# Kernel optimization log

Hardware: AMD Instinct MI355X
Metric: run time of the kernel (lower is better)

The kernel has to match this reference:

```python
import jax, jax.numpy as jnp
import numpy as np

B, O, A, H, Z = 4096, 512, 64, 2048, 256
CLAMP = 10.0


def _lin(x, w, b):
    # torch nn.Linear layout: w [out, in]
    return x @ w.T + b


def setup_inputs() -> dict:
    key = jax.random.key(0)
    ks = jax.random.split(key, 24)
    n = jax.random.normal
    s = 0.02
    inp = {
        'x_t': n(ks[0], (B, O), jnp.float32),
        'a_prev': n(ks[1], (B, A), jnp.float32),
        'h_prev': n(ks[2], (B, H), jnp.float32),
        'eps': n(ks[3], (B, Z), jnp.float32),
        # prior_net: Linear(H,H) -> ReLU -> Linear(H, 2Z)
        'prior_w1': n(ks[4], (H, H), jnp.float32) * s,
        'prior_b1': jnp.zeros((H,), jnp.float32),
        'prior_w2': n(ks[5], (2 * Z, H), jnp.float32) * s,
        'prior_b2': jnp.zeros((2 * Z,), jnp.float32),
        # enc_net: Linear(O+H,H) -> ReLU -> Linear(H, 2Z)
        'enc_w1': n(ks[6], (H, O + H), jnp.float32) * s,
        'enc_b1': jnp.zeros((H,), jnp.float32),
        'enc_w2': n(ks[7], (2 * Z, H), jnp.float32) * s,
        'enc_b2': jnp.zeros((2 * Z,), jnp.float32),
        # dec_net: Linear(Z+H,H) -> ReLU -> Linear(H, 2O)
        'dec_w1': n(ks[8], (H, Z + H), jnp.float32) * s,
        'dec_b1': jnp.zeros((H,), jnp.float32),
        'dec_w2': n(ks[9], (2 * O, H), jnp.float32) * s,
        'dec_b2': jnp.zeros((2 * O,), jnp.float32),
        # GRUCell: input = O + A + Z, gates ordered (r, z, n)
        'w_ih': n(ks[10], (3 * H, O + A + Z), jnp.float32) * s,
        'w_hh': n(ks[11], (3 * H, H), jnp.float32) * s,
        'b_ih': jnp.zeros((3 * H,), jnp.float32),
        'b_hh': jnp.zeros((3 * H,), jnp.float32),
    }
    return inp


def vrnn_step(x_t, a_prev, h_prev, eps,
              prior_w1, prior_b1, prior_w2, prior_b2,
              enc_w1, enc_b1, enc_w2, enc_b2,
              dec_w1, dec_b1, dec_w2, dec_b2,
              w_ih, w_hh, b_ih, b_hh):
    # prior stats from h_prev
    prior_stats = _lin(jax.nn.relu(_lin(h_prev, prior_w1, prior_b1)), prior_w2, prior_b2)
    mu_p, logvar_p = jnp.split(prior_stats, 2, axis=-1)

    # encoder on [x, h]
    enc_stats = _lin(jax.nn.relu(_lin(jnp.concatenate([x_t, h_prev], -1), enc_w1, enc_b1)), enc_w2, enc_b2)
    mu_q, logvar_q = jnp.split(enc_stats, 2, axis=-1)
    logvar_q = jnp.clip(logvar_q, -CLAMP, CLAMP)
    std_q = jnp.exp(0.5 * logvar_q)
    z_t = mu_q + eps * std_q  # reparameterization

    # decoder on [z, h]
    dec_out = _lin(jax.nn.relu(_lin(jnp.concatenate([z_t, h_prev], -1), dec_w1, dec_b1)), dec_w2, dec_b2)
    mu_x, logvar_x = jnp.split(dec_out, 2, axis=-1)
    logvar_x = jnp.clip(logvar_x, -CLAMP, CLAMP)
    nll = 0.5 * jnp.sum((x_t - mu_x) ** 2 * jnp.exp(-logvar_x) + logvar_x, axis=-1)

    # KL(q || p), diagonal Gaussians
    var_p = jnp.exp(logvar_p)
    kl = 0.5 * jnp.sum((mu_q - mu_p) ** 2 / var_p + jnp.exp(logvar_q) / var_p
                       + (logvar_p - logvar_q) - 1.0, axis=-1)

    # GRUCell (torch gate order: r, z, n)
    rnn_in = jnp.concatenate([x_t, z_t, a_prev], -1)
    gi = rnn_in @ w_ih.T + b_ih
    gh = h_prev @ w_hh.T + b_hh
    i_r, i_z, i_n = jnp.split(gi, 3, axis=-1)
    h_r, h_z, h_n = jnp.split(gh, 3, axis=-1)
    r = jax.nn.sigmoid(i_r + h_r)
    zg = jax.nn.sigmoid(i_z + h_z)
    n = jnp.tanh(i_n + r * h_n)
    h_t = (1.0 - zg) * n + zg * h_prev

    return h_t, nll, kl, z_t, mu_q, logvar_q


def reference(x_t, a_prev, h_prev, eps,
              prior_w1, prior_b1, prior_w2, prior_b2,
              enc_w1, enc_b1, enc_w2, enc_b2,
              dec_w1, dec_b1, dec_w2, dec_b2,
              w_ih, w_hh, b_ih, b_hh):
    return vrnn_step(x_t, a_prev, h_prev, eps,
                     prior_w1, prior_b1, prior_w2, prior_b2,
                     enc_w1, enc_b1, enc_w2, enc_b2,
                     dec_w1, dec_b1, dec_w2, dec_b2,
                     w_ih, w_hh, b_ih, b_hh)
```

## Files before the change

kernel.cpp:

```cpp
#include <hip/hip_runtime.h>
#include <stdint.h>


#define B_SZ 4096
#define H_SZ 2048
#define Z_SZ 256

typedef __attribute__((ext_vector_type(4))) float f32x4;
typedef __attribute__((ext_vector_type(8))) short s16x8;

__device__ __forceinline__ uint16_t f2b(float f) {
  union { float f; uint32_t u; } v; v.f = f;
  uint32_t u = v.u;
  uint32_t r = (u + 0x7FFFu + ((u >> 16) & 1u)) >> 16;
  return (uint16_t)r;
}
__device__ __forceinline__ float b2f(uint16_t h) {
  union { uint32_t u; float f; } v; v.u = ((uint32_t)h) << 16; return v.f;
}
__device__ __forceinline__ float clip10(float v) { return fminf(fmaxf(v, -10.0f), 10.0f); }

struct MC {
  const float* src[14];
  uint16_t* dst[14];
  int c8[14];
  int sld[14];
  int dld[14];
  int base[15];
};

__global__ __launch_bounds__(256) void multiconv(MC mc, int nseg, int total) {
  int gid = blockIdx.x * 256 + threadIdx.x;
  if (gid >= total) return;
  int s = 0;
  while (s + 1 < nseg && gid >= mc.base[s + 1]) ++s;
  int local = gid - mc.base[s];
  int c8 = mc.c8[s];
  int row = local / c8;
  int cg = local - row * c8;
  const f32x4* sp = (const f32x4*)(mc.src[s] + (size_t)row * mc.sld[s] + (size_t)cg * 8);
  f32x4 lo = sp[0], hi = sp[1];
  s16x8 p;
  p[0] = (short)f2b(lo[0]); p[1] = (short)f2b(lo[1]);
  p[2] = (short)f2b(lo[2]); p[3] = (short)f2b(lo[3]);
  p[4] = (short)f2b(hi[0]); p[5] = (short)f2b(hi[1]);
  p[6] = (short)f2b(hi[2]); p[7] = (short)f2b(hi[3]);
  *(s16x8*)(mc.dst[s] + (size_t)row * mc.dld[s] + (size_t)cg * 8) = p;
}

__global__ void biascat_kernel(const float* __restrict__ b0, const float* __restrict__ b1,
                               const float* __restrict__ b2, const float* __restrict__ b3,
                               float* __restrict__ dst) {
  int j = blockIdx.x * 256 + threadIdx.x;
  float v;
  if (j < 2048) v = b0[j];
  else if (j < 8192) v = b1[j - 2048];
  else if (j < 10240) v = b2[j - 8192];
  else v = b3[j - 10240];
  dst[j] = v;
}

__device__ __forceinline__ void gload_lds16(const uint16_t* g, uint16_t* l) {
  __builtin_amdgcn_global_load_lds(
      (const __attribute__((address_space(1))) uint32_t*)g,
      (__attribute__((address_space(3))) uint32_t*)(uintptr_t)(void*)l,
      16, 0, 0);
}

__global__ __launch_bounds__(512, 2)
void gemm8p(const uint16_t* __restrict__ A, int lda,
            const uint16_t* __restrict__ W,
            const float* __restrict__ bias,
            uint16_t* __restrict__ C, int ldc, int splitN,
            int Nt, int K) {
  __shared__ uint16_t Ab[2][2][8192];
  __shared__ uint16_t Bb[2][2][8192];
  const int NT = K >> 6;
  int mtile = blockIdx.x / Nt;
  int ntile = blockIdx.x - mtile * Nt;
  const int brow = mtile << 8, bcol = ntile << 8;
  const int tid = threadIdx.x;
  const int l = tid & 63;
  const int w = tid >> 6;
  const int wr = w >> 2, wcn = w & 3;
  const int fr = l & 15, fq = l >> 4;
  const int sr0 = tid >> 3;
  const int scg = tid & 7;
  const int dstoff = tid * 8;

  f32x4 acc[8][4] = {};

  auto stage_half = [&](int t, int q, int d) {
#pragma unroll
    for (int r = 0; r < 2; ++r) {
      int row = r * 64 + sr0;
      int col = (scg ^ (row & 7)) << 3;
      if (q < 2)
        gload_lds16(A + (size_t)(brow + q * 128 + row) * lda + t * 64 + col,
                    &Ab[d][q][r * 4096 + dstoff]);
      else
        gload_lds16(W + (size_t)(bcol + (q - 2) * 128 + row) * K + t * 64 + col,
                    &Bb[d][q - 2][r * 4096 + dstoff]);
    }
  };

#pragma unroll
  for (int q = 0; q < 4; ++q) stage_half(0, q, 0);

  for (int t = 0; t < NT; ++t) {
    const int d = t & 1;
    const bool more = (t + 1 < NT);
    if (more) {
      stage_half(t + 1, 0, d ^ 1);
      asm volatile("s_waitcnt vmcnt(2)" ::: "memory");
    } else {
      asm volatile("s_waitcnt vmcnt(0)" ::: "memory");
    }
    __builtin_amdgcn_s_barrier();

#pragma unroll
    for (int q = 0; q < 4; ++q) {
      const int mh = q >> 1, nh = q & 1;
      if (q > 0 && more) stage_half(t + 1, q, d ^ 1);
      s16x8 fb[2][2];
#pragma unroll
      for (int nn = 0; nn < 2; ++nn)
#pragma unroll
        for (int ks = 0; ks < 2; ++ks) {
          int row = wcn * 64 + nh * 32 + nn * 16 + fr;
          int half = row >> 7, rl = row & 127;
          fb[nn][ks] = *(const s16x8*)&Bb[d][half]
              [rl * 64 + ((ks * 32 + fq * 8) ^ ((rl & 7) << 3))];
        }
      s16x8 fa[4][2];
#pragma unroll
      for (int mm = 0; mm < 4; ++mm)
#pragma unroll
        for (int ks = 0; ks < 2; ++ks) {
          int rl = mh * 64 + mm * 16 + fr;
          fa[mm][ks] = *(const s16x8*)&Ab[d][wr]
              [rl * 64 + ((ks * 32 + fq * 8) ^ ((rl & 7) << 3))];
        }
      __builtin_amdgcn_s_setprio(1);
#pragma unroll
      for (int mm = 0; mm < 4; ++mm)
#pragma unroll
        for (int nn = 0; nn < 2; ++nn)
#pragma unroll
          for (int ks = 0; ks < 2; ++ks)
            acc[mh * 4 + mm][nh * 2 + nn] = __builtin_amdgcn_mfma_f32_16x16x32_bf16(
                fa[mm][ks], fb[nn][ks], acc[mh * 4 + mm][nh * 2 + nn], 0, 0, 0);
      __builtin_amdgcn_s_setprio(0);
      __builtin_amdgcn_s_barrier();
    }
  }

#pragma unroll
  for (int m = 0; m < 8; ++m) {
    int grow = brow + wr * 128 + m * 16 + fq * 4;
#pragma unroll
    for (int n = 0; n < 4; ++n) {
      int gcol = bcol + wcn * 64 + n * 16 + fr;
      float bs = bias[gcol];
      bool doRelu = gcol < splitN;
#pragma unroll
      for (int i = 0; i < 4; ++i) {
        float v = acc[m][n][i] + bs;
        if (doRelu) v = fmaxf(v, 0.0f);
        C[(size_t)(grow + i) * ldc + gcol] = f2b(v);
      }
    }
  }
}

template <int EPI>
__global__ __launch_bounds__(256)
void gemm_bt(const uint16_t* __restrict__ A0, int lda0, int ks1,
             const uint16_t* __restrict__ A1, int lda1, int ks2,
             const uint16_t* __restrict__ A2, int lda2,
             const uint16_t* __restrict__ W,
             const float* __restrict__ bias0, const float* __restrict__ bias1,
             uint16_t* __restrict__ C0, int ldc0, int splitN,
             uint16_t* __restrict__ C1, int ldc1,
             int Nt, int K) {
  __shared__ uint16_t As[128 * 64];
  __shared__ uint16_t Ws[128 * 64];
  int mtile = blockIdx.x / Nt;
  int ntile = blockIdx.x - mtile * Nt;
  const int row0 = mtile << 7, col0 = ntile << 7;
  const int t = threadIdx.x;
  const int w = t >> 6, l = t & 63;
  const int wr = w >> 1, wc = w & 1;
  const int sr = l >> 3, scg = l & 7;
  const int fr = l & 15, fq = l >> 4;

  f32x4 acc[4][4] = {};

  const uint16_t* Wbase = W + (size_t)(col0 + w * 32 + sr) * K + scg * 8;

  for (int k0 = 0; k0 < K; k0 += 64) {
    const uint16_t* ab; int ald, koff;
    if (k0 < ks1)      { ab = A0; ald = lda0; koff = k0; }
    else if (k0 < ks2) { ab = A1; ald = lda1; koff = k0 - ks1; }
    else               { ab = A2; ald = lda2; koff = k0 - ks2; }
    const uint16_t* Abase = ab + (size_t)(row0 + w * 32 + sr) * ald + koff + scg * 8;
#pragma unroll
    for (int j = 0; j < 4; ++j)
      gload_lds16(Abase + (size_t)(j * 8) * ald, &As[(w * 32 + j * 8) * 64]);
#pragma unroll
    for (int j = 0; j < 4; ++j)
      gload_lds16(Wbase + (size_t)(j * 8) * K + k0, &Ws[(w * 32 + j * 8) * 64]);
    __syncthreads();
#pragma unroll
    for (int ks = 0; ks < 2; ++ks) {
      s16x8 fa[4], fb[4];
#pragma unroll
      for (int m = 0; m < 4; ++m)
        fa[m] = *(const s16x8*)&As[(wr * 64 + m * 16 + fr) * 64 + ks * 32 + fq * 8];
#pragma unroll
      for (int n = 0; n < 4; ++n)
        fb[n] = *(const s16x8*)&Ws[(wc * 64 + n * 16 + fr) * 64 + ks * 32 + fq * 8];
#pragma unroll
      for (int m = 0; m < 4; ++m)
#pragma unroll
        for (int n = 0; n < 4; ++n)
          acc[m][n] = __builtin_amdgcn_mfma_f32_16x16x32_bf16(fa[m], fb[n], acc[m][n], 0, 0, 0);
    }
    __syncthreads();
  }

#pragma unroll
  for (int m = 0; m < 4; ++m) {
    int grow = row0 + wr * 64 + m * 16 + fq * 4;
#pragma unroll
    for (int n = 0; n < 4; ++n) {
      int gcol = col0 + wc * 64 + n * 16 + fr;
      bool first = (EPI != 3) || (gcol < splitN);
      float bs = first ? bias0[gcol] : bias1[gcol - splitN];
#pragma unroll
      for (int i = 0; i < 4; ++i) {
        size_t idx0 = (size_t)(grow + i) * ldc0 + gcol;
        if (EPI == 6) {
          float v6 = acc[m][n][i] + b2f(C0[idx0]);
          C0[idx0] = f2b(fmaxf(v6, 0.0f));
        } else {
          float v = acc[m][n][i] + bs;
          if (EPI == 1 || (EPI == 3 && first)) v = fmaxf(v, 0.0f);
          if (first)
            C0[idx0] = f2b(v);
          else
            C1[(size_t)(grow + i) * ldc1 + (gcol - splitN)] = f2b(v);
        }
      }
    }
  }
}

__global__ __launch_bounds__(256)
void gemm_ks(const uint16_t* __restrict__ A, int lda,
             const uint16_t* __restrict__ W, int Wld,
             float* __restrict__ P, int N,
             int Nt, int Khalf) {
  __shared__ uint16_t As[128 * 64];
  __shared__ uint16_t Ws[128 * 64];
  int bg = gridDim.x >> 1;
  int half = blockIdx.x >= bg;
  int bid = blockIdx.x - half * bg;
  int mtile = bid / Nt;
  int ntile = bid - mtile * Nt;
  const int row0 = mtile << 7, col0 = ntile << 7;
  const int t = threadIdx.x;
  const int w = t >> 6, l = t & 63;
  const int wr = w >> 1, wc = w & 1;
  const int sr = l >> 3, scg = l & 7;
  const int fr = l & 15, fq = l >> 4;

  f32x4 acc[4][4] = {};

  const uint16_t* Ab = A + half * Khalf;
  const uint16_t* Wb = W + half * Khalf;
  const uint16_t* Wbase = Wb + (size_t)(col0 + w * 32 + sr) * Wld + scg * 8;
  const uint16_t* Abase0 = Ab + (size_t)(row0 + w * 32 + sr) * lda + scg * 8;

  for (int k0 = 0; k0 < Khalf; k0 += 64) {
#pragma unroll
    for (int j = 0; j < 4; ++j)
      gload_lds16(Abase0 + (size_t)(j * 8) * lda + k0, &As[(w * 32 + j * 8) * 64]);
#pragma unroll
    for (int j = 0; j < 4; ++j)
      gload_lds16(Wbase + (size_t)(j * 8) * Wld + k0, &Ws[(w * 32 + j * 8) * 64]);
    __syncthreads();
#pragma unroll
    for (int ks = 0; ks < 2; ++ks) {
      s16x8 fa[4], fb[4];
#pragma unroll
      for (int m = 0; m < 4; ++m)
        fa[m] = *(const s16x8*)&As[(wr * 64 + m * 16 + fr) * 64 + ks * 32 + fq * 8];
#pragma unroll
      for (int n = 0; n < 4; ++n)
        fb[n] = *(const s16x8*)&Ws[(wc * 64 + n * 16 + fr) * 64 + ks * 32 + fq * 8];
#pragma unroll
      for (int m = 0; m < 4; ++m)
#pragma unroll
        for (int n = 0; n < 4; ++n)
          acc[m][n] = __builtin_amdgcn_mfma_f32_16x16x32_bf16(fa[m], fb[n], acc[m][n], 0, 0, 0);
    }
    __syncthreads();
  }

  float* Pf = P + (size_t)half * B_SZ * N;
#pragma unroll
  for (int m = 0; m < 4; ++m) {
    int grow = row0 + wr * 64 + m * 16 + fq * 4;
#pragma unroll
    for (int n = 0; n < 4; ++n) {
      int gcol = col0 + wc * 64 + n * 16 + fr;
#pragma unroll
      for (int i = 0; i < 4; ++i)
        Pf[(size_t)(grow + i) * N + gcol] = acc[m][n][i];
    }
  }
}

__global__ __launch_bounds__(256)
void gemm_ks2(const uint16_t* __restrict__ Aa, const uint16_t* __restrict__ Ab2,
              int lda,
              const uint16_t* __restrict__ Wa, const uint16_t* __restrict__ Wb2,
              int Wld,
              float* __restrict__ P, int N,
              int Nt, int Khalf) {
  __shared__ uint16_t As[128 * 64];
  __shared__ uint16_t Ws[128 * 64];
  int bg2 = gridDim.x >> 1;
  int pair = blockIdx.x >= bg2;
  int bidp = blockIdx.x - pair * bg2;
  int bg = bg2 >> 1;
  int half = bidp >= bg;
  int bid = bidp - half * bg;
  int mtile = bid / Nt;
  int ntile = bid - mtile * Nt;
  const int row0 = mtile << 7, col0 = ntile << 7;
  const int t = threadIdx.x;
  const int w = t >> 6, l = t & 63;
  const int wr = w >> 1, wc = w & 1;
  const int sr = l >> 3, scg = l & 7;
  const int fr = l & 15, fq = l >> 4;

  f32x4 acc[4][4] = {};

  const uint16_t* A = pair ? Ab2 : Aa;
  const uint16_t* W = pair ? Wb2 : Wa;
  const uint16_t* Ab = A + half * Khalf;
  const uint16_t* Wb = W + half * Khalf;
  const uint16_t* Wbase = Wb + (size_t)(col0 + w * 32 + sr) * Wld + scg * 8;
  const uint16_t* Abase0 = Ab + (size_t)(row0 + w * 32 + sr) * lda + scg * 8;

  for (int k0 = 0; k0 < Khalf; k0 += 64) {
#pragma unroll
    for (int j = 0; j < 4; ++j)
      gload_lds16(Abase0 + (size_t)(j * 8) * lda + k0, &As[(w * 32 + j * 8) * 64]);
#pragma unroll
    for (int j = 0; j < 4; ++j)
      gload_lds16(Wbase + (size_t)(j * 8) * Wld + k0, &Ws[(w * 32 + j * 8) * 64]);
    __syncthreads();
#pragma unroll
    for (int ks = 0; ks < 2; ++ks) {
      s16x8 fa[4], fb[4];
#pragma unroll
      for (int m = 0; m < 4; ++m)
        fa[m] = *(const s16x8*)&As[(wr * 64 + m * 16 + fr) * 64 + ks * 32 + fq * 8];
#pragma unroll
      for (int n = 0; n < 4; ++n)
        fb[n] = *(const s16x8*)&Ws[(wc * 64 + n * 16 + fr) * 64 + ks * 32 + fq * 8];
#pragma unroll
      for (int m = 0; m < 4; ++m)
#pragma unroll
        for (int n = 0; n < 4; ++n)
          acc[m][n] = __builtin_amdgcn_mfma_f32_16x16x32_bf16(fa[m], fb[n], acc[m][n], 0, 0, 0);
    }
    __syncthreads();
  }

  float* Pf = P + (size_t)pair * 2 * B_SZ * N + (size_t)half * B_SZ * N;
#pragma unroll
  for (int m = 0; m < 4; ++m) {
    int grow = row0 + wr * 64 + m * 16 + fq * 4;
#pragma unroll
    for (int n = 0; n < 4; ++n) {
      int gcol = col0 + wc * 64 + n * 16 + fr;
#pragma unroll
      for (int i = 0; i < 4; ++i)
        Pf[(size_t)(grow + i) * N + gcol] = acc[m][n][i];
    }
  }
}

__global__ __launch_bounds__(256)
void combine2(const float* __restrict__ P, const float* __restrict__ bias,
              uint16_t* __restrict__ dst, int N, int total4) {
  int i = blockIdx.x * 256 + threadIdx.x;
  if (i >= total4) return;
  size_t idx = (size_t)i * 4;
  const float* P1 = P + (size_t)B_SZ * N;
  f32x4 a = *(const f32x4*)(P + idx);
  f32x4 b = *(const f32x4*)(P1 + idx);
  int col = (int)(idx & (size_t)(N - 1));
#pragma unroll
  for (int k = 0; k < 4; ++k)
    dst[idx + k] = f2b(a[k] + b[k] + bias[col + k]);
}

__global__ __launch_bounds__(256)
void combine2z(const float* __restrict__ P, const float* __restrict__ bias,
               const float* __restrict__ eps,
               uint16_t* __restrict__ estats,
               float* __restrict__ oz, float* __restrict__ omu, float* __restrict__ olq,
               uint16_t* __restrict__ xza) {
  int i = blockIdx.x * 256 + threadIdx.x;
  int b = i >> 8, j = i & 255;
  const float* P1 = P + (size_t)B_SZ * 512;
  size_t i0 = (size_t)b * 512 + j;
  size_t i1 = i0 + 256;
  float mu = P[i0] + P1[i0] + bias[j];
  float lq = P[i1] + P1[i1] + bias[j + 256];
  estats[i0] = f2b(mu);
  estats[i1] = f2b(lq);
  float lqc = clip10(lq);
  float z = mu + eps[i] * __expf(0.5f * lqc);
  oz[i] = z; omu[i] = mu; olq[i] = lqc;
  xza[(size_t)b * 832 + 512 + j] = f2b(z);
}

__device__ __forceinline__ float block_sum256(float v) {
  __shared__ float ps[4];
#pragma unroll
  for (int o = 32; o > 0; o >>= 1) v += __shfl_xor(v, o, 64);
  int l = threadIdx.x & 63, w = threadIdx.x >> 6;
  if (l == 0) ps[w] = v;
  __syncthreads();
  float r = ps[0] + ps[1] + ps[2] + ps[3];
  __syncthreads();
  return r;
}

__global__ __launch_bounds__(256)
void gru_fused_t1(const uint16_t* __restrict__ gi, int ldgi,
                  const uint16_t* __restrict__ gh, int ldgh,
                  const float* __restrict__ hp, const float* __restrict__ x,
                  const uint16_t* __restrict__ dec, const uint16_t* __restrict__ pst,
                  const uint16_t* __restrict__ es,
                  float* __restrict__ out_h, float* __restrict__ out_nll,
                  float* __restrict__ out_kl) {
  int b = blockIdx.x, t = threadIdx.x;
  size_t gbi = (size_t)b * ldgi + (size_t)t * 8;
  size_t gbh = (size_t)b * ldgh + (size_t)t * 8;
  s16x8 ir = *(const s16x8*)(gi + gbi);
  s16x8 iz = *(const s16x8*)(gi + gbi + 2048);
  s16x8 inn = *(const s16x8*)(gi + gbi + 4096);
  s16x8 hr = *(const s16x8*)(gh + gbh);
  s16x8 hz = *(const s16x8*)(gh + gbh + 2048);
  s16x8 hn = *(const s16x8*)(gh + gbh + 4096);
  size_t hbase = (size_t)b * 2048 + (size_t)t * 8;
  f32x4 h0 = *(const f32x4*)(hp + hbase);
  f32x4 h1v = *(const f32x4*)(hp + hbase + 4);
  f32x4 o0, o1;
#pragma unroll
  for (int e = 0; e < 8; ++e) {
    float r = 1.f / (1.f + __expf(-(b2f((uint16_t)ir[e]) + b2f((uint16_t)hr[e]))));
    float zg = 1.f / (1.f + __expf(-(b2f((uint16_t)iz[e]) + b2f((uint16_t)hz[e]))));
    float nv = b2f((uint16_t)inn[e]) + r * b2f((uint16_t)hn[e]);
    float t2 = __expf(-2.f * fabsf(nv));
    float n = (1.f - t2) / (1.f + t2);
    n = (nv >= 0.f) ? n : -n;
    float hv = (e < 4) ? h0[e] : h1v[e - 4];
    float o = (1.f - zg) * n + zg * hv;
    if (e < 4) o0[e] = o; else o1[e - 4] = o;
  }
  *(f32x4*)(out_h + hbase) = o0;
  *(f32x4*)(out_h + hbase + 4) = o1;

  float s = 0.f;
#pragma unroll
  for (int rr = 0; rr < 2; ++rr) {
    int j = t + rr * 256;
    float mu = b2f(dec[(size_t)b * 1024 + j]);
    float lx = clip10(b2f(dec[(size_t)b * 1024 + 512 + j]));
    float d = x[(size_t)b * 512 + j] - mu;
    s += d * d * __expf(-lx) + lx;
  }
  s = block_sum256(s);
  if (t == 0) out_nll[b] = 0.5f * s;

  float mu_p = b2f(pst[(size_t)b * 512 + t]);
  float lp = b2f(pst[(size_t)b * 512 + 256 + t]);
  float mu_q = b2f(es[(size_t)b * 512 + t]);
  float lq = clip10(b2f(es[(size_t)b * 512 + 256 + t]));
  float dq = mu_q - mu_p;
  float enl = __expf(-lp);
  float kv = dq * dq * enl + __expf(lq) * enl + (lp - lq) - 1.0f;
  kv = block_sum256(kv);
  if (t == 0) out_kl[b] = 0.5f * kv;
}

template <int MODE>
__global__ __launch_bounds__(256)
void gemm_nv(const float* __restrict__ A0, int ld0, int s1,
             const float* __restrict__ A1, int ld1, int s2,
             const float* __restrict__ A2, int ld2,
             const float* __restrict__ W, const float* __restrict__ bias,
             float* __restrict__ C, int N, int K) {
  int nb = N >> 8;
  int m = blockIdx.x / nb;
  int n = (blockIdx.x - m * nb) * 256 + threadIdx.x;
  const float* w = W + (size_t)n * K;
  float acc = 0.f;
  int k = 0;
  for (; k < s1; ++k) acc += A0[(size_t)m * ld0 + k] * w[k];
  for (; k < s2; ++k) acc += A1[(size_t)m * ld1 + (k - s1)] * w[k];
  for (; k < K; ++k) acc += A2[(size_t)m * ld2 + (k - s2)] * w[k];
  acc += bias[n];
  if (MODE == 1) acc = fmaxf(acc, 0.f);
  C[(size_t)m * N + n] = acc;
}

__global__ void z_nv(const float* __restrict__ ests, const float* __restrict__ eps,
                     float* __restrict__ oz, float* __restrict__ omu,
                     float* __restrict__ olq, float* __restrict__ zs, int row0, int nR) {
  int i = blockIdx.x * 256 + threadIdx.x;
  if (i >= nR * 256) return;
  int bl = i >> 8, j = i & 255;
  size_t g = (size_t)(row0 + bl) * 256 + j;
  float mu = ests[(size_t)bl * 512 + j];
  float lq = clip10(ests[(size_t)bl * 512 + 256 + j]);
  float z = mu + eps[g] * __expf(0.5f * lq);
  oz[g] = z; omu[g] = mu; olq[g] = lq;
  zs[(size_t)bl * 256 + j] = z;
}

__global__ void nll_nv(const float* __restrict__ x, const float* __restrict__ decs,
                       float* __restrict__ out, int row0) {
  int bl = blockIdx.x, l = threadIdx.x;
  int gb = row0 + bl;
  float s = 0.f;
  for (int j = l; j < 512; j += 64) {
    float mu = decs[(size_t)bl * 1024 + j];
    float lx = clip10(decs[(size_t)bl * 1024 + 512 + j]);
    float d = x[(size_t)gb * 512 + j] - mu;
    s += d * d * __expf(-lx) + lx;
  }
#pragma unroll
  for (int o = 32; o > 0; o >>= 1) s += __shfl_xor(s, o, 64);
  if (l == 0) out[gb] = 0.5f * s;
}

__global__ void kl_nv(const float* __restrict__ psts, const float* __restrict__ ests,
                      float* __restrict__ out, int row0) {
  int bl = blockIdx.x, l = threadIdx.x;
  int gb = row0 + bl;
  float s = 0.f;
  for (int j = l; j < 256; j += 64) {
    float mu_p = psts[(size_t)bl * 512 + j];
    float lp = psts[(size_t)bl * 512 + 256 + j];
    float mu_q = ests[(size_t)bl * 512 + j];
    float lq = clip10(ests[(size_t)bl * 512 + 256 + j]);
    float d = mu_q - mu_p;
    float enl = __expf(-lp);
    s += d * d * enl + __expf(lq) * enl + (lp - lq) - 1.0f;
  }
#pragma unroll
  for (int o = 32; o > 0; o >>= 1) s += __shfl_xor(s, o, 64);
  if (l == 0) out[gb] = 0.5f * s;
}

__global__ void gru_nv(const float* __restrict__ gis, const float* __restrict__ ghs,
                       const float* __restrict__ hp, float* __restrict__ ho,
                       int row0, int nR) {
  int i = blockIdx.x * 256 + threadIdx.x;
  if (i >= nR * 2048) return;
  int bl = i >> 11, j = i & 2047;
  size_t lb = (size_t)bl * 6144 + j;
  float r = 1.f / (1.f + __expf(-(gis[lb] + ghs[lb])));
  float zg = 1.f / (1.f + __expf(-(gis[lb + 2048] + ghs[lb + 2048])));
  float nv = gis[lb + 4096] + r * ghs[lb + 4096];
  float t2 = __expf(-2.f * fabsf(nv));
  float n = (1.f - t2) / (1.f + t2);
  n = (nv >= 0.f) ? n : -n;
  size_t g = (size_t)(row0 + bl) * 2048 + j;
  ho[g] = (1.f - zg) * n + zg * hp[g];
}

extern "C" void kernel_launch(void* const* d_in, const int* in_sizes, int n_in,
                              void* d_out, int out_size, void* d_ws, size_t ws_size,
                              hipStream_t stream) {
  const float* x_t = (const float*)d_in[0];
  const float* a_prev = (const float*)d_in[1];
  const float* h_prev = (const float*)d_in[2];
  const float* eps = (const float*)d_in[3];
  const float* prior_w1 = (const float*)d_in[4];
  const float* prior_b1 = (const float*)d_in[5];
  const float* prior_w2 = (const float*)d_in[6];
  const float* prior_b2 = (const float*)d_in[7];
  const float* enc_w1 = (const float*)d_in[8];
  const float* enc_b1 = (const float*)d_in[9];
  const float* enc_w2 = (const float*)d_in[10];
  const float* enc_b2 = (const float*)d_in[11];
  const float* dec_w1 = (const float*)d_in[12];
  const float* dec_b1 = (const float*)d_in[13];
  const float* dec_w2 = (const float*)d_in[14];
  const float* dec_b2 = (const float*)d_in[15];
  const float* w_ih = (const float*)d_in[16];
  const float* w_hh = (const float*)d_in[17];
  const float* b_ih = (const float*)d_in[18];
  const float* b_hh = (const float*)d_in[19];

  float* out = (float*)d_out;
  float* out_h = out;
  float* out_nll = out + (size_t)B_SZ * H_SZ;
  float* out_kl = out_nll + B_SZ;
  float* out_z = out_kl + B_SZ;
  float* out_mu = out_z + (size_t)B_SZ * Z_SZ;
  float* out_lq = out_mu + (size_t)B_SZ * Z_SZ;

  char* ws = (char*)d_ws;
  size_t off = 0;
  auto alloc = [&](size_t bytes) {
    void* p = ws + off;
    off += (bytes + 255) & ~(size_t)255;
    return p;
  };

  const size_t T1_DEMAND = 196500000;

  if (ws_size >= T1_DEMAND) {
    uint16_t* wmega = (uint16_t*)alloc((size_t)12288 * 2048 * 2);
    uint16_t* wih = (uint16_t*)alloc((size_t)6144 * 832 * 2);
    uint16_t* wx_enc = (uint16_t*)alloc((size_t)2048 * 512 * 2);
    uint16_t* wz_dec = (uint16_t*)alloc((size_t)2048 * 256 * 2);
    uint16_t* pw2 = (uint16_t*)alloc((size_t)512 * 2048 * 2);
    uint16_t* ew2 = (uint16_t*)alloc((size_t)512 * 2048 * 2);
    uint16_t* dw2 = (uint16_t*)alloc((size_t)1024 * 2048 * 2);
    uint16_t* xza = (uint16_t*)alloc((size_t)B_SZ * 832 * 2);
    uint16_t* hbuf = (uint16_t*)alloc((size_t)B_SZ * 2048 * 2);
    uint16_t* megaC = (uint16_t*)alloc((size_t)B_SZ * 12288 * 2);
    float* biascat = (float*)alloc(12288 * 4);
    float* Pbuf = (float*)wmega;
    uint16_t* gi = wmega;
    uint16_t* pstats = hbuf;
    uint16_t* estats = hbuf + (size_t)2097152;
    uint16_t* decout = pw2;

    MC mc;
    int nseg = 0, acc = 0;
    auto seg = [&](const float* s, uint16_t* d, int R, int C, int sld, int dld) {
      mc.src[nseg] = s; mc.dst[nseg] = d; mc.c8[nseg] = C / 8;
      mc.sld[nseg] = sld; mc.dld[nseg] = dld; mc.base[nseg] = acc;
      acc += R * (C / 8); ++nseg;
    };
    seg(prior_w1, wmega, 2048, 2048, 2048, 2048);
    seg(w_hh, wmega + (size_t)2048 * 2048, 6144, 2048, 2048, 2048);
    seg(enc_w1 + 512, wmega + (size_t)8192 * 2048, 2048, 2048, 2560, 2048);
    seg(dec_w1 + 256, wmega + (size_t)10240 * 2048, 2048, 2048, 2304, 2048);
    seg(enc_w1, wx_enc, 2048, 512, 2560, 512);
    seg(dec_w1, wz_dec, 2048, 256, 2304, 256);
    seg(prior_w2, pw2, 512, 2048, 2048, 2048);
    seg(enc_w2, ew2, 512, 2048, 2048, 2048);
    seg(dec_w2, dw2, 1024, 2048, 2048, 2048);
    seg(w_ih, wih, 6144, 832, 832, 832);
    seg(x_t, xza, B_SZ, 512, 512, 832);
    seg(a_prev, xza + 768, B_SZ, 64, 64, 832);
    seg(h_prev, hbuf, B_SZ, 2048, 2048, 2048);
    mc.base[nseg] = acc;
    multiconv<<<dim3((acc + 255) / 256), dim3(256), 0, stream>>>(mc, nseg, acc);
    biascat_kernel<<<dim3(48), dim3(256), 0, stream>>>(prior_b1, b_hh, enc_b1, dec_b1, biascat);

    gemm8p<<<dim3((B_SZ / 256) * 48), dim3(512), 0, stream>>>(
        hbuf, 2048, wmega, biascat, megaC, 12288, 2048, 48, 2048);
    gemm_bt<6><<<dim3((B_SZ / 128) * 16), dim3(256), 0, stream>>>(
        xza, 832, 512, xza, 832, 512, xza, 832, wx_enc,
        enc_b1, enc_b1, megaC + 8192, 12288, 2048, megaC + 8192, 12288, 16, 512);
    gemm_ks2<<<dim3((B_SZ / 128) * 4 * 2 * 2), dim3(256), 0, stream>>>(
        megaC, megaC + 8192, 12288, pw2, ew2, 2048, Pbuf, 512, 4, 1024);
    combine2<<<dim3(B_SZ * 512 / 4 / 256), dim3(256), 0, stream>>>(
        Pbuf, prior_b2, pstats, 512, B_SZ * 512 / 4);
    combine2z<<<dim3(B_SZ * Z_SZ / 256), dim3(256), 0, stream>>>(
        Pbuf + (size_t)2 * B_SZ * 512, enc_b2, eps, estats,
        out_z, out_mu, out_lq, xza);
    gemm_bt<6><<<dim3((B_SZ / 128) * 16), dim3(256), 0, stream>>>(
        xza + 512, 832, 256, xza + 512, 832, 256, xza + 512, 832, wz_dec,
        dec_b1, dec_b1, megaC + 10240, 12288, 2048, megaC + 10240, 12288, 16, 256);
    gemm_ks<<<dim3((B_SZ / 128) * 8 * 2), dim3(256), 0, stream>>>(
        megaC + 10240, 12288, dw2, 2048, Pbuf, 1024, 8, 1024);
    combine2<<<dim3(B_SZ * 1024 / 4 / 256), dim3(256), 0, stream>>>(
        Pbuf, dec_b2, decout, 1024, B_SZ * 1024 / 4);
    gemm_bt<2><<<dim3((B_SZ / 128) * 48), dim3(256), 0, stream>>>(
        xza, 832, 832, xza, 832, 832, xza, 832, wih,
        b_ih, b_ih, gi, 6144, 6144, gi, 6144, 48, 832);
    gru_fused_t1<<<dim3(B_SZ), dim3(256), 0, stream>>>(
        gi, 6144, megaC + 2048, 12288, h_prev, x_t, decout, pstats, estats,
        out_h, out_nll, out_kl);
  } else {
    int R = 512;
    while (R > 32 && (size_t)R * 66560 + 4096 > ws_size) R >>= 1;
    float* h1s = (float*)alloc((size_t)R * 2048 * 4);
    float* psts = (float*)alloc((size_t)R * 512 * 4);
    float* ests = (float*)alloc((size_t)R * 512 * 4);
    float* decs = (float*)alloc((size_t)R * 1024 * 4);
    float* zs = (float*)alloc((size_t)R * 256 * 4);
    float* gis = (float*)alloc((size_t)R * 6144 * 4);
    float* ghs = (float*)alloc((size_t)R * 6144 * 4);
    const float* dummy = x_t;

    auto nv = [&](const float* A0, int ld0, int s1, const float* A1, int ld1, int s2,
                  const float* A2, int ld2, const float* W, const float* bias,
                  float* C, int M, int N, int K, int relu) {
      dim3 grid(M * (N / 256));
      if (relu)
        gemm_nv<1><<<grid, dim3(256), 0, stream>>>(A0, ld0, s1, A1, ld1, s2, A2, ld2, W, bias, C, N, K);
      else
        gemm_nv<0><<<grid, dim3(256), 0, stream>>>(A0, ld0, s1, A1, ld1, s2, A2, ld2, W, bias, C, N, K);
    };

    for (int s = 0; s < B_SZ / R; ++s) {
      int r0 = s * R;
      const float* xs = x_t + (size_t)r0 * 512;
      const float* hs = h_prev + (size_t)r0 * 2048;
      const float* as = a_prev + (size_t)r0 * 64;
      nv(hs, 2048, 2048, dummy, 0, 2048, dummy, 0, prior_w1, prior_b1, h1s, R, 2048, 2048, 1);
      nv(h1s, 2048, 2048, dummy, 0, 2048, dummy, 0, prior_w2, prior_b2, psts, R, 512, 2048, 0);
      nv(xs, 512, 512, hs, 2048, 2560, dummy, 0, enc_w1, enc_b1, h1s, R, 2048, 2560, 1);
      nv(h1s, 2048, 2048, dummy, 0, 2048, dummy, 0, enc_w2, enc_b2, ests, R, 512, 2048, 0);
      z_nv<<<dim3((R * 256 + 255) / 256), dim3(256), 0, stream>>>(
          ests, eps, out_z, out_mu, out_lq, zs, r0, R);
      nv(zs, 256, 256, hs, 2048, 2304, dummy, 0, dec_w1, dec_b1, h1s, R, 2048, 2304, 1);
      nv(h1s, 2048, 2048, dummy, 0, 2048, dummy, 0, dec_w2, dec_b2, decs, R, 1024, 2048, 0);
      nv(hs, 2048, 2048, dummy, 0, 2048, dummy, 0, w_hh, b_hh, ghs, R, 6144, 2048, 0);
      nv(xs, 512, 512, zs, 256, 768, as, 64, w_ih, b_ih, gis, R, 6144, 832, 0);
      nll_nv<<<dim3(R), dim3(64), 0, stream>>>(x_t, decs, out_nll, r0);
      kl_nv<<<dim3(R), dim3(64), 0, stream>>>(psts, ests, out_kl, r0);
      gru_nv<<<dim3((R * 2048 + 255) / 256), dim3(256), 0, stream>>>(
          gis, ghs, h_prev, out_h, r0, R);
    }
  }
}
```

Measured before the change: 460.3 us.

## Stage gemm8p epilogue through LDS for vectorized stores; merge prior/encoder combine kernels

```diff
diff --git a/kernel.cpp b/kernel.cpp
--- a/kernel.cpp
+++ b/kernel.cpp
@@ -155,21 +155,41 @@
     }
   }
 
-#pragma unroll
-  for (int m = 0; m < 8; ++m) {
-    int grow = brow + wr * 128 + m * 16 + fq * 4;
-#pragma unroll
-    for (int n = 0; n < 4; ++n) {
-      int gcol = bcol + wcn * 64 + n * 16 + fr;
-      float bs = bias[gcol];
-      bool doRelu = gcol < splitN;
-#pragma unroll
-      for (int i = 0; i < 4; ++i) {
-        float v = acc[m][n][i] + bs;
-        if (doRelu) v = fmaxf(v, 0.0f);
-        C[(size_t)(grow + i) * ldc + gcol] = f2b(v);
+  {
+    uint16_t* wbuf = &Ab[0][0][0] + w * 2176;
+    const int wb_lane = fq * (4 * 68) + fr * 2;
+#pragma unroll
+    for (int pp = 0; pp < 4; ++pp) {
+      asm volatile("s_waitcnt lgkmcnt(0)" ::: "memory");
+      __builtin_amdgcn_sched_barrier(0);
+#pragma unroll
+      for (int mi = 0; mi < 2; ++mi) {
+        int m = pp * 2 + mi;
+#pragma unroll
+        for (int n = 0; n < 4; ++n) {
+          int gcol = bcol + wcn * 64 + n * 16 + fr;
+          float bs = bias[gcol];
+          bool doRelu = gcol < splitN;
+#pragma unroll
+          for (int i = 0; i < 4; ++i) {
+            float v = acc[m][n][i] + bs;
+            if (doRelu) v = fmaxf(v, 0.0f);
+            wbuf[(mi * 16 + fq * 4 + i) * 68 + n * 16 + fr] = f2b(v);
+          }
+        }
       }
-    }
+      asm volatile("s_waitcnt lgkmcnt(0)" ::: "memory");
+      __builtin_amdgcn_sched_barrier(0);
+#pragma unroll
+      for (int j = 0; j < 4; ++j) {
+        int lrow = j * 8 + (l >> 3);
+        s16x8 vv = *(const s16x8*)&wbuf[lrow * 68 + (l & 7) * 8];
+        int grow = brow + wr * 128 + pp * 32 + lrow;
+        int gcol8 = bcol + wcn * 64 + (l & 7) * 8;
+        *(s16x8*)&C[(size_t)grow * ldc + gcol8] = vv;
+      }
+    }
+    (void)wb_lane;
   }
 }
 
@@ -411,24 +431,37 @@
 }
 
 __global__ __launch_bounds__(256)
-void combine2z(const float* __restrict__ P, const float* __restrict__ bias,
-               const float* __restrict__ eps,
-               uint16_t* __restrict__ estats,
-               float* __restrict__ oz, float* __restrict__ omu, float* __restrict__ olq,
-               uint16_t* __restrict__ xza) {
-  int i = blockIdx.x * 256 + threadIdx.x;
-  int b = i >> 8, j = i & 255;
-  const float* P1 = P + (size_t)B_SZ * 512;
-  size_t i0 = (size_t)b * 512 + j;
-  size_t i1 = i0 + 256;
-  float mu = P[i0] + P1[i0] + bias[j];
-  float lq = P[i1] + P1[i1] + bias[j + 256];
-  estats[i0] = f2b(mu);
-  estats[i1] = f2b(lq);
-  float lqc = clip10(lq);
-  float z = mu + eps[i] * __expf(0.5f * lqc);
-  oz[i] = z; omu[i] = mu; olq[i] = lqc;
-  xza[(size_t)b * 832 + 512 + j] = f2b(z);
+void combine_pe(const float* __restrict__ P, const float* __restrict__ pbias,
+                const float* __restrict__ ebias, const float* __restrict__ eps,
+                uint16_t* __restrict__ pstats, uint16_t* __restrict__ estats,
+                float* __restrict__ oz, float* __restrict__ omu,
+                float* __restrict__ olq, uint16_t* __restrict__ xza) {
+  if (blockIdx.x < 2048) {
+    int i = blockIdx.x * 256 + threadIdx.x;
+    size_t idx = (size_t)i * 4;
+    const float* P1 = P + (size_t)B_SZ * 512;
+    f32x4 a = *(const f32x4*)(P + idx);
+    f32x4 b = *(const f32x4*)(P1 + idx);
+    int col = (int)(idx & 511);
+#pragma unroll
+    for (int k = 0; k < 4; ++k)
+      pstats[idx + k] = f2b(a[k] + b[k] + pbias[col + k]);
+  } else {
+    int i = (blockIdx.x - 2048) * 256 + threadIdx.x;
+    int b = i >> 8, j = i & 255;
+    const float* E0 = P + (size_t)2 * B_SZ * 512;
+    const float* E1 = E0 + (size_t)B_SZ * 512;
+    size_t i0 = (size_t)b * 512 + j;
+    size_t i1 = i0 + 256;
+    float mu = E0[i0] + E1[i0] + ebias[j];
+    float lq = E0[i1] + E1[i1] + ebias[j + 256];
+    estats[i0] = f2b(mu);
+    estats[i1] = f2b(lq);
+    float lqc = clip10(lq);
+    float z = mu + eps[i] * __expf(0.5f * lqc);
+    oz[i] = z; omu[i] = mu; olq[i] = lqc;
+    xza[(size_t)b * 832 + 512 + j] = f2b(z);
+  }
 }
 
 __device__ __forceinline__ float block_sum256(float v) {
@@ -680,10 +713,8 @@
         enc_b1, enc_b1, megaC + 8192, 12288, 2048, megaC + 8192, 12288, 16, 512);
     gemm_ks2<<<dim3((B_SZ / 128) * 4 * 2 * 2), dim3(256), 0, stream>>>(
         megaC, megaC + 8192, 12288, pw2, ew2, 2048, Pbuf, 512, 4, 1024);
-    combine2<<<dim3(B_SZ * 512 / 4 / 256), dim3(256), 0, stream>>>(
-        Pbuf, prior_b2, pstats, 512, B_SZ * 512 / 4);
-    combine2z<<<dim3(B_SZ * Z_SZ / 256), dim3(256), 0, stream>>>(
-        Pbuf + (size_t)2 * B_SZ * 512, enc_b2, eps, estats,
+    combine_pe<<<dim3(6144), dim3(256), 0, stream>>>(
+        Pbuf, prior_b2, enc_b2, eps, pstats, estats,
         out_z, out_mu, out_lq, xza);
     gemm_bt<6><<<dim3((B_SZ / 128) * 16), dim3(256), 0, stream>>>(
         xza + 512, 832, 256, xza + 512, 832, 256, xza + 512, 832, wz_dec,
```

After: 463.5 us. No clear change (+0.7%).
